# Optimization experiments

Hardware: AMD Instinct MI355X
Metric: run time of the kernel (lower is better)

Reference implementation:

```python
import jax, jax.numpy as jnp
import numpy as np

B, K, S, L, D, A = 16, 128, 64, 2, 256, 500  # batch, beam, stack, layers, hidden, max_actions


def setup_inputs() -> dict:
    key = jax.random.key(0)
    k = jax.random.split(key, 8)
    return {
        "gen_ll": jax.random.normal(k[0], (B, K), jnp.float32),
        "trees": jax.random.normal(k[1], (B, K, S, D), jnp.float32),
        "hiddens": jax.random.normal(k[2], (B, K, S + 1, L, D), jnp.float32),
        "cells": jax.random.normal(k[3], (B, K, S + 1, L, D), jnp.float32),
        "actions": jax.random.randint(k[4], (B, K, A), 0, 100, dtype=jnp.int64)
        if jax.config.jax_enable_x64 else jax.random.randint(k[4], (B, K, A), 0, 100),
        "actions_pos": jax.random.randint(k[5], (B, K), 0, A - 1),
        "pointer": jax.random.randint(k[6], (B, K), 0, S),
        "beam_widths": jax.random.randint(k[7], (B,), 1, K + 1),  # >= 1 active beam per batch
    }


def _gather_beam(x, sort_idx):
    # gather along beam dim (axis=1) with broadcast over trailing dims
    idx = sort_idx.reshape(sort_idx.shape + (1,) * (x.ndim - 2))
    return jnp.take_along_axis(x, idx, axis=1)


def reference(gen_ll, trees, hiddens, cells, actions, actions_pos, pointer, beam_widths):
    # BeamItems.shrink(): mask beams outside active width, sort by score desc,
    # then reorder every parallel tensor (stack + action path) by sort_idx.
    order = jnp.arange(K)
    active = order[None, :] < beam_widths[:, None]                    # [B, K] active_idx_mask
    gen_ll_m = jnp.where(active, gen_ll, -jnp.inf)
    sort_idx = jnp.argsort(-gen_ll_m, axis=1)                          # descending sort
    gen_ll_s = jnp.take_along_axis(gen_ll_m, sort_idx, axis=1)

    trees_s = _gather_beam(trees, sort_idx)                            # stack.sort_by
    hiddens_s = _gather_beam(hiddens, sort_idx)
    cells_s = _gather_beam(cells, sort_idx)
    actions_s = _gather_beam(actions, sort_idx)                        # action_path.sort_by
    actions_pos_s = jnp.take_along_axis(actions_pos, sort_idx, axis=1)
    pointer_s = jnp.take_along_axis(pointer, sort_idx, axis=1)         # stack_state.sort_by

    new_beam_widths = jnp.minimum(beam_widths, K)
    # BeamItems.marginal_probs(): logsumexp over active beams (inactive already -inf)
    marginal = jax.nn.logsumexp(gen_ll_s, axis=1)                      # [B]
    # ActionPath.prev_actions(): gather at actions_pos
    prev_actions = jnp.take_along_axis(actions_s, actions_pos_s[:, :, None], axis=2)[:, :, 0]

    return (gen_ll_s, trees_s, hiddens_s, cells_s, marginal,
            actions_s, actions_pos_s, pointer_s, prev_actions, new_beam_widths)
```

## Files before the change

### kernel.cpp

```cpp
#include <hip/hip_runtime.h>
#include <math.h>

#define B 16
#define K 128
#define S 64
#define L 2
#define D 256
#define A 500

#define ROW4_TREES 4096
#define HALF4_HID  4160

#define NEG_BIG (-1.0e30f)

typedef float f32x4 __attribute__((ext_vector_type(4)));
typedef int   i32x4 __attribute__((ext_vector_type(4)));

#define OFF_GENLL 0
#define OFF_TREES 2048
#define OFF_HID   33556480
#define OFF_CELLS 101713920
#define OFF_MARG  169871360
#define OFF_ACT   169871376
#define OFF_APOS  170895376
#define OFF_PTR   170897424
#define OFF_PREV  170899472
#define OFF_NBW   170901520

#define NU_TREES 2048
#define GRID (NU_TREES + 8192)

template<int N4>
__device__ __forceinline__ void copy_unit(const f32x4* __restrict__ s,
                                          f32x4* __restrict__ d, int tid)
{
    constexpr int FULL = N4 / 256;
    constexpr int REM  = N4 % 256;
    for (int g = 0; g < FULL; g += 8) {
        f32x4 v[8];
#pragma unroll
        for (int i = 0; i < 8; ++i)
            v[i] = __builtin_nontemporal_load(&s[(g + i) * 256 + tid]);
#pragma unroll
        for (int i = 0; i < 8; ++i)
            __builtin_nontemporal_store(v[i], &d[(g + i) * 256 + tid]);
    }
    if (REM && tid < REM) {
        f32x4 v = __builtin_nontemporal_load(&s[FULL * 256 + tid]);
        __builtin_nontemporal_store(v, &d[FULL * 256 + tid]);
    }
}

__global__ void __launch_bounds__(256, 8)
k_fused(const float* __restrict__ gen_ll,
        const f32x4* __restrict__ trees,
        const f32x4* __restrict__ hiddens,
        const f32x4* __restrict__ cells,
        const int* __restrict__ actions,
        const int* __restrict__ actions_pos,
        const int* __restrict__ pointer,
        const int* __restrict__ beam_widths,
        float* __restrict__ out)
{
    __shared__ float key[K];
    __shared__ int   sidx[K];
    __shared__ float red[4];

    const int tid = threadIdx.x;
    const int bid = blockIdx.x;

    int b, k;
    int which = -1, u3 = 0;
    if (bid < NU_TREES) {
        b = bid >> 7; k = bid & 127;
    } else {
        const int u2 = bid - NU_TREES;
        which = u2 >> 12;
        u3 = u2 & 4095;
        const int row = u3 >> 1;
        b = row >> 7; k = row & 127;
    }

    const int w = beam_widths[b];
    if (tid < K) key[tid] = (tid < w) ? gen_ll[b * K + tid] : NEG_BIG;
    __syncthreads();
    if (tid < K) {
        const float my = key[tid];
        int rank = 0;
#pragma unroll 16
        for (int i = 0; i < K; ++i) {
            const float ki = key[i];
            rank += (ki > my) || (ki == my && i < tid);
        }
        sidx[rank] = tid;
    }
    __syncthreads();

    const int j = sidx[k];

    if (which < 0) {
        copy_unit<ROW4_TREES>(trees + (size_t)(b * K + j) * ROW4_TREES,
                              (f32x4*)(out + OFF_TREES) + (size_t)bid * ROW4_TREES,
                              tid);
        {
            const i32x4* s = (const i32x4*)actions + (size_t)(b * K + j) * 125;
            f32x4* d = (f32x4*)(out + OFF_ACT) + (size_t)bid * 125;
            if (tid < 125) {
                const i32x4 v = __builtin_nontemporal_load(&s[tid]);
                f32x4 f;
                f.x = (float)v.x; f.y = (float)v.y; f.z = (float)v.z; f.w = (float)v.w;
                __builtin_nontemporal_store(f, &d[tid]);
            }
        }
        if (k == 0) {
            if (tid < K) {
                const int jj = sidx[tid];
                out[OFF_GENLL + b * K + tid] = key[jj];
                const int ap = actions_pos[b * K + jj];
                out[OFF_APOS + b * K + tid] = (float)ap;
                out[OFF_PTR  + b * K + tid] = (float)pointer[b * K + jj];
                out[OFF_PREV + b * K + tid] = (float)actions[(size_t)(b * K + jj) * A + ap];
            }
            const float v = (tid < K) ? key[tid] : NEG_BIG;
            if (tid < 128) {
                float m = v;
#pragma unroll
                for (int mask = 32; mask >= 1; mask >>= 1)
                    m = fmaxf(m, __shfl_xor(m, mask, 64));
                if ((tid & 63) == 0) red[tid >> 6] = m;
            }
            __syncthreads();
            const float m = fmaxf(red[0], red[1]);
            if (tid < 128) {
                float e = expf(v - m);
#pragma unroll
                for (int mask = 32; mask >= 1; mask >>= 1)
                    e += __shfl_xor(e, mask, 64);
                if ((tid & 63) == 0) red[2 + (tid >> 6)] = e;
            }
            __syncthreads();
            if (tid == 0) {
                out[OFF_MARG + b] = m + logf(red[2] + red[3]);
                out[OFF_NBW + b] = (float)(w < K ? w : K);
            }
        }
    } else {
        const int half = u3 & 1;
        const f32x4* src = (which ? cells : hiddens)
                         + ((size_t)(b * K + j) * 2 + half) * HALF4_HID;
        f32x4* dst = (f32x4*)(out + (which ? OFF_CELLS : OFF_HID))
                   + (size_t)u3 * HALF4_HID;
        copy_unit<HALF4_HID>(src, dst, tid);
    }
}

extern "C" void kernel_launch(void* const* d_in, const int* in_sizes, int n_in,
                              void* d_out, int out_size, void* d_ws, size_t ws_size,
                              hipStream_t stream)
{
    const float* gen_ll      = (const float*)d_in[0];
    const float* trees       = (const float*)d_in[1];
    const float* hiddens     = (const float*)d_in[2];
    const float* cells       = (const float*)d_in[3];
    const int*   actions     = (const int*)d_in[4];
    const int*   actions_pos = (const int*)d_in[5];
    const int*   pointer     = (const int*)d_in[6];
    const int*   beam_widths = (const int*)d_in[7];
    float* out = (float*)d_out;

    k_fused<<<GRID, 256, 0, stream>>>(gen_ll, (const f32x4*)trees,
                                      (const f32x4*)hiddens, (const f32x4*)cells,
                                      actions, actions_pos, pointer, beam_widths, out);
}
```

Baseline: 256.0 us.

## Switch to scatter by inverse rank and prefetch source rows before sorting

Result: no change. 252.8 us (-1.3%).

```diff
diff --git a/kernel.cpp b/kernel.cpp
--- a/kernel.cpp
+++ b/kernel.cpp
@@ -30,27 +30,6 @@
 #define NU_TREES 2048
 #define GRID (NU_TREES + 8192)
 
-template<int N4>
-__device__ __forceinline__ void copy_unit(const f32x4* __restrict__ s,
-                                          f32x4* __restrict__ d, int tid)
-{
-    constexpr int FULL = N4 / 256;
-    constexpr int REM  = N4 % 256;
-    for (int g = 0; g < FULL; g += 8) {
-        f32x4 v[8];
-#pragma unroll
-        for (int i = 0; i < 8; ++i)
-            v[i] = __builtin_nontemporal_load(&s[(g + i) * 256 + tid]);
-#pragma unroll
-        for (int i = 0; i < 8; ++i)
-            __builtin_nontemporal_store(v[i], &d[(g + i) * 256 + tid]);
-    }
-    if (REM && tid < REM) {
-        f32x4 v = __builtin_nontemporal_load(&s[FULL * 256 + tid]);
-        __builtin_nontemporal_store(v, &d[FULL * 256 + tid]);
-    }
-}
-
 __global__ void __launch_bounds__(256, 8)
 k_fused(const float* __restrict__ gen_ll,
         const f32x4* __restrict__ trees,
@@ -64,22 +43,31 @@
 {
     __shared__ float key[K];
     __shared__ int   sidx[K];
+    __shared__ int   rnk[K];
     __shared__ float red[4];
 
     const int tid = threadIdx.x;
     const int bid = blockIdx.x;
 
-    int b, k;
-    int which = -1, u3 = 0;
+    int b, k, which = -1, half = 0;
     if (bid < NU_TREES) {
         b = bid >> 7; k = bid & 127;
     } else {
         const int u2 = bid - NU_TREES;
         which = u2 >> 12;
-        u3 = u2 & 4095;
+        const int u3 = u2 & 4095;
+        half = u3 & 1;
         const int row = u3 >> 1;
         b = row >> 7; k = row & 127;
     }
+
+    const f32x4* s = (which < 0)
+        ? trees + (size_t)(b * K + k) * ROW4_TREES
+        : (which ? cells : hiddens) + ((size_t)(b * K + k) * 2 + half) * HALF4_HID;
+    f32x4 v[8];
+#pragma unroll
+    for (int i = 0; i < 8; ++i)
+        v[i] = __builtin_nontemporal_load(&s[i * 256 + tid]);
 
     const int w = beam_widths[b];
     if (tid < K) key[tid] = (tid < w) ? gen_ll[b * K + tid] : NEG_BIG;
@@ -93,25 +81,35 @@
             rank += (ki > my) || (ki == my && i < tid);
         }
         sidx[rank] = tid;
+        rnk[tid] = rank;
     }
     __syncthreads();
 
-    const int j = sidx[k];
+    const int rr = rnk[k];
 
     if (which < 0) {
-        copy_unit<ROW4_TREES>(trees + (size_t)(b * K + j) * ROW4_TREES,
-                              (f32x4*)(out + OFF_TREES) + (size_t)bid * ROW4_TREES,
-                              tid);
+        f32x4* d = (f32x4*)(out + OFF_TREES) + (size_t)((b << 7) + rr) * ROW4_TREES;
+#pragma unroll
+        for (int i = 0; i < 8; ++i)
+            __builtin_nontemporal_store(v[i], &d[i * 256 + tid]);
+#pragma unroll
+        for (int i = 0; i < 8; ++i)
+            v[i] = __builtin_nontemporal_load(&s[(8 + i) * 256 + tid]);
+#pragma unroll
+        for (int i = 0; i < 8; ++i)
+            __builtin_nontemporal_store(v[i], &d[(8 + i) * 256 + tid]);
+
         {
-            const i32x4* s = (const i32x4*)actions + (size_t)(b * K + j) * 125;
-            f32x4* d = (f32x4*)(out + OFF_ACT) + (size_t)bid * 125;
+            const i32x4* sa = (const i32x4*)actions + (size_t)(b * K + k) * 125;
+            f32x4* da = (f32x4*)(out + OFF_ACT) + (size_t)((b << 7) + rr) * 125;
             if (tid < 125) {
-                const i32x4 v = __builtin_nontemporal_load(&s[tid]);
+                const i32x4 av = __builtin_nontemporal_load(&sa[tid]);
                 f32x4 f;
-                f.x = (float)v.x; f.y = (float)v.y; f.z = (float)v.z; f.w = (float)v.w;
-                __builtin_nontemporal_store(f, &d[tid]);
+                f.x = (float)av.x; f.y = (float)av.y; f.z = (float)av.z; f.w = (float)av.w;
+                __builtin_nontemporal_store(f, &da[tid]);
             }
         }
+
         if (k == 0) {
             if (tid < K) {
                 const int jj = sidx[tid];
@@ -121,9 +119,9 @@
                 out[OFF_PTR  + b * K + tid] = (float)pointer[b * K + jj];
                 out[OFF_PREV + b * K + tid] = (float)actions[(size_t)(b * K + jj) * A + ap];
             }
-            const float v = (tid < K) ? key[tid] : NEG_BIG;
+            const float vv = (tid < K) ? key[tid] : NEG_BIG;
             if (tid < 128) {
-                float m = v;
+                float m = vv;
 #pragma unroll
                 for (int mask = 32; mask >= 1; mask >>= 1)
                     m = fmaxf(m, __shfl_xor(m, mask, 64));
@@ -132,7 +130,7 @@
             __syncthreads();
             const float m = fmaxf(red[0], red[1]);
             if (tid < 128) {
-                float e = expf(v - m);
+                float e = expf(vv - m);
 #pragma unroll
                 for (int mask = 32; mask >= 1; mask >>= 1)
                     e += __shfl_xor(e, mask, 64);
@@ -145,12 +143,21 @@
             }
         }
     } else {
-        const int half = u3 & 1;
-        const f32x4* src = (which ? cells : hiddens)
-                         + ((size_t)(b * K + j) * 2 + half) * HALF4_HID;
-        f32x4* dst = (f32x4*)(out + (which ? OFF_CELLS : OFF_HID))
-                   + (size_t)u3 * HALF4_HID;
-        copy_unit<HALF4_HID>(src, dst, tid);
+        f32x4* d = (f32x4*)(out + (which ? OFF_CELLS : OFF_HID))
+                 + ((size_t)((b << 7) + rr) * 2 + half) * HALF4_HID;
+#pragma unroll
+        for (int i = 0; i < 8; ++i)
+            __builtin_nontemporal_store(v[i], &d[i * 256 + tid]);
+#pragma unroll
+        for (int i = 0; i < 8; ++i)
+            v[i] = __builtin_nontemporal_load(&s[(8 + i) * 256 + tid]);
+#pragma unroll
+        for (int i = 0; i < 8; ++i)
+            __builtin_nontemporal_store(v[i], &d[(8 + i) * 256 + tid]);
+        if (tid < 64) {
+            const f32x4 t = __builtin_nontemporal_load(&s[16 * 256 + tid]);
+            __builtin_nontemporal_store(t, &d[16 * 256 + tid]);
+        }
     }
 }
 
```
